# Kernel tuning notes

Measured on AMD Instinct MI355X. Metric: run time of the kernel, lower is better.

The kernel has to match this reference:

```python
import jax, jax.numpy as jnp
import numpy as np

K_BITS = 128  # hash bits (k in __init__)
WORD = 32     # pack bits into uint32 words -> K_BITS // WORD = 4 words


def _pack_bits(bits_u32):
    # bits_u32: [N, K_BITS] uint32 in {0,1} -> [N, K_BITS//WORD] uint32 keys
    N = bits_u32.shape[0]
    b = bits_u32.reshape(N, K_BITS // WORD, WORD)
    shifts = jnp.arange(WORD, dtype=jnp.uint32)
    return jnp.sum(jnp.left_shift(b, shifts), axis=-1, dtype=jnp.uint32)  # [N, 4]


def setup_inputs() -> dict:
    key = jax.random.key(0)
    k1, k2 = jax.random.split(key)
    T, B, D = 128, 64, 4096
    latent_state = jax.random.normal(k1, (T, B, D), dtype=jnp.float32)
    A = jax.random.normal(k2, (K_BITS, D), dtype=jnp.float32)  # fixed random projection buffer
    return {"latent_state": latent_state, "A": A}


def reference(latent_state, A):
    # latent_state: [T, B, D]; A: [k, D]. Returns intrinsic reward [T, B].
    T, B, D = latent_state.shape
    flat = latent_state.reshape(T * B, D)                    # detach is a no-op for fwd
    proj = flat @ A.T                                        # [N, k]
    bits = (proj > 0).astype(jnp.uint32)                     # SimHash sign bits
    words = _pack_bits(bits)                                 # [N, 4] collision-free 128-bit key

    # counts dict starts empty each run: visit count of row i is the number of
    # rows j <= i with an identical key (keys processed in row order).
    N = words.shape[0]
    eq = jnp.ones((N, N), dtype=bool)
    for w in range(K_BITS // WORD):  # small fixed loop over 4 key words
        eq = eq & (words[:, None, w] == words[None, :, w])
    counts = jnp.tril(eq).sum(axis=1)                        # [N] int, >= 1
    intrinsic = 1.0 / jnp.sqrt(counts.astype(latent_state.dtype))
    return intrinsic.reshape(T, B)
```

## Files before the change

### kernel.cpp

```cpp
#include <hip/hip_runtime.h>
#include <stdint.h>

#define D_DIM 4096
#define N_ROWS 8192

typedef __attribute__((ext_vector_type(8))) short bfrag8;
typedef __attribute__((ext_vector_type(4))) float facc4;

__device__ __forceinline__ uint32_t pack_bf16x2(float lo, float hi) {
    union { float f; uint32_t u; } a, b;
    a.f = lo; b.f = hi;
    return (b.u & 0xFFFF0000u) | (a.u >> 16);
}

__global__ void __launch_bounds__(256)
prep_A(const float* __restrict__ A, uint32_t* __restrict__ A_sw) {
    const int S = blockIdx.x * 256 + threadIdx.x;
    const int c = S >> 10;
    const int s = S & 1023;
    const int n = s >> 3;
    const int g = (s & 7) ^ (n & 7);
    const float* src = A + (size_t)n * D_DIM + c * 64 + g * 8;
    float4 f0 = *(const float4*)(src);
    float4 f1 = *(const float4*)(src + 4);
    uint4 o;
    o.x = pack_bf16x2(f0.x, f0.y);
    o.y = pack_bf16x2(f0.z, f0.w);
    o.z = pack_bf16x2(f1.x, f1.y);
    o.w = pack_bf16x2(f1.z, f1.w);
    *(uint4*)(A_sw + (size_t)S * 4) = o;
}

__global__ void __launch_bounds__(256)
gemm_pack(const float* __restrict__ L, const uint32_t* __restrict__ A_sw,
          unsigned long long* __restrict__ folded) {
    __shared__ ushort Ls[32 * 72];
    __shared__ uint4 As[1024];
    __shared__ unsigned long long halves[2][32];

    const int tid  = threadIdx.x;
    const int wave = tid >> 6;
    const int lane = tid & 63;
    const int row0 = blockIdx.x * 32;
    const int c  = lane & 15;
    const int q  = lane >> 4;
    const int wm = wave >> 1;
    const int wn = wave & 1;

    const int lrow = tid >> 3;
    const int lf4  = tid & 7;
    const float* lsrc = L + (size_t)(row0 + lrow) * D_DIM + lf4 * 4;
    ushort* ldst = &Ls[lrow * 72 + lf4 * 4];

    facc4 acc[4];
#pragma unroll
    for (int i = 0; i < 4; i++) acc[i] = (facc4){0.f, 0.f, 0.f, 0.f};

    for (int kc = 0; kc < D_DIM; kc += 64) {
        const uint32_t* gA = A_sw + (size_t)(kc >> 6) * 4096;
#pragma unroll
        for (int i = 0; i < 4; i++) {
            const int slot0 = wave * 256 + i * 64;
            __builtin_amdgcn_global_load_lds(
                (const __attribute__((address_space(1))) uint32_t*)(gA + (slot0 + lane) * 4),
                (__attribute__((address_space(3))) uint32_t*)(&As[slot0]),
                16, 0, 0);
        }
        float4 f0 = *(const float4*)(lsrc + kc);
        float4 f1 = *(const float4*)(lsrc + kc + 32);
        *(uint2*)ldst        = make_uint2(pack_bf16x2(f0.x, f0.y), pack_bf16x2(f0.z, f0.w));
        *(uint2*)(ldst + 32) = make_uint2(pack_bf16x2(f1.x, f1.y), pack_bf16x2(f1.z, f1.w));
        __syncthreads();

#pragma unroll
        for (int ks = 0; ks < 2; ks++) {
            bfrag8 a = *(const bfrag8*)&Ls[(16 * wm + c) * 72 + ks * 32 + q * 8];
#pragma unroll
            for (int ct = 0; ct < 4; ct++) {
                const int n  = 64 * wn + 16 * ct + c;
                const int gl = ks * 4 + q;
                bfrag8 b = *(const bfrag8*)&As[n * 8 + (gl ^ (n & 7))];
                acc[ct] = __builtin_amdgcn_mfma_f32_16x16x32_bf16(a, b, acc[ct], 0, 0, 0);
            }
        }
        __syncthreads();
    }

    unsigned long long masks[4][4];
#pragma unroll
    for (int ct = 0; ct < 4; ct++)
#pragma unroll
        for (int r = 0; r < 4; r++)
            masks[ct][r] = __ballot(acc[ct][r] > 0.0f);

    if (lane < 16) {
        const int qq = lane >> 2, r = lane & 3;
        unsigned long long half = 0;
#pragma unroll
        for (int ct = 0; ct < 4; ct++) {
            unsigned long long bits = (masks[ct][r] >> (16 * qq)) & 0xFFFFull;
            half |= bits << (16 * ct);
        }
        halves[wn][16 * wm + lane] = half;
    }
    __syncthreads();
    if (tid < 32)
        folded[row0 + tid] = halves[0][tid] ^ halves[1][tid];
}

__global__ void __launch_bounds__(256)
count_rows(const unsigned long long* __restrict__ folded, float* __restrict__ out) {
    const int row  = (blockIdx.x << 2) + (threadIdx.x >> 6);
    const int lane = threadIdx.x & 63;
    const unsigned long long my = folded[row];
    int cnt = 0;
    for (int j = lane; j <= row; j += 64)
        cnt += (folded[j] == my);
#pragma unroll
    for (int o = 32; o; o >>= 1) cnt += __shfl_xor(cnt, o, 64);
    if (lane == 0) out[row] = rsqrtf((float)cnt);
}

extern "C" void kernel_launch(void* const* d_in, const int* in_sizes, int n_in,
                              void* d_out, int out_size, void* d_ws, size_t ws_size,
                              hipStream_t stream) {
    const float* latent = (const float*)d_in[0];
    const float* A      = (const float*)d_in[1];
    float* out          = (float*)d_out;

    uint32_t* A_sw = (uint32_t*)d_ws;
    unsigned long long* folded = (unsigned long long*)((char*)d_ws + (1 << 20));

    prep_A<<<256, 256, 0, stream>>>(A, A_sw);
    gemm_pack<<<256, 256, 0, stream>>>(latent, A_sw, folded);
    count_rows<<<2048, 256, 0, stream>>>(folded, out);
}
```

Baseline: 256.0 us.

## Split GEMM over K across blocks and batch collision counting through LDS

Adds a split-K GEMM path. S blocks per 32-row tile write float partial projections to workspace, and a reduce kernel sums them, takes the sign bits and folds them into a key. The aim is to fill the GPU, which the 256-block launch leaves underused. The counting kernel is also rewritten: it stages all keys in LDS and has each wave handle four rows spread across the triangle, for shared loads and better load balance. The cost is extra global traffic for the partials (up to 32 MB) and one extra kernel launch. The split path only runs if the workspace is large enough.

Measured after the change: 226.3 us. -11.6%, faster.

```diff
diff --git a/kernel.cpp b/kernel.cpp
--- a/kernel.cpp
+++ b/kernel.cpp
@@ -6,6 +6,7 @@
 
 typedef __attribute__((ext_vector_type(8))) short bfrag8;
 typedef __attribute__((ext_vector_type(4))) float facc4;
+typedef unsigned long long u64;
 
 __device__ __forceinline__ uint32_t pack_bf16x2(float lo, float hi) {
     union { float f; uint32_t u; } a, b;
@@ -32,11 +33,93 @@
 }
 
 __global__ void __launch_bounds__(256)
-gemm_pack(const float* __restrict__ L, const uint32_t* __restrict__ A_sw,
-          unsigned long long* __restrict__ folded) {
+gemm_split(const float* __restrict__ L, const uint32_t* __restrict__ A_sw,
+           float* __restrict__ partials, int kpb) {
     __shared__ ushort Ls[32 * 72];
     __shared__ uint4 As[1024];
-    __shared__ unsigned long long halves[2][32];
+
+    const int tid  = threadIdx.x;
+    const int wave = tid >> 6;
+    const int lane = tid & 63;
+    const int split = blockIdx.x;
+    const int row0 = blockIdx.y * 32;
+    const int c  = lane & 15;
+    const int q  = lane >> 4;
+    const int wm = wave >> 1;
+    const int wn = wave & 1;
+
+    const int lrow = tid >> 3;
+    const int lf4  = tid & 7;
+    const float* lsrc = L + (size_t)(row0 + lrow) * D_DIM + lf4 * 4;
+    ushort* ldst = &Ls[lrow * 72 + lf4 * 4];
+
+    facc4 acc[4];
+#pragma unroll
+    for (int i = 0; i < 4; i++) acc[i] = (facc4){0.f, 0.f, 0.f, 0.f};
+
+    const int kc0 = split * kpb * 64;
+    const int kc1 = kc0 + kpb * 64;
+    for (int kc = kc0; kc < kc1; kc += 64) {
+        const uint32_t* gA = A_sw + (size_t)(kc >> 6) * 4096;
+#pragma unroll
+        for (int i = 0; i < 4; i++) {
+            const int slot0 = wave * 256 + i * 64;
+            __builtin_amdgcn_global_load_lds(
+                (const __attribute__((address_space(1))) uint32_t*)(gA + (slot0 + lane) * 4),
+                (__attribute__((address_space(3))) uint32_t*)(&As[slot0]),
+                16, 0, 0);
+        }
+        float4 f0 = *(const float4*)(lsrc + kc);
+        float4 f1 = *(const float4*)(lsrc + kc + 32);
+        *(uint2*)ldst        = make_uint2(pack_bf16x2(f0.x, f0.y), pack_bf16x2(f0.z, f0.w));
+        *(uint2*)(ldst + 32) = make_uint2(pack_bf16x2(f1.x, f1.y), pack_bf16x2(f1.z, f1.w));
+        __syncthreads();
+
+#pragma unroll
+        for (int ks = 0; ks < 2; ks++) {
+            bfrag8 a = *(const bfrag8*)&Ls[(16 * wm + c) * 72 + ks * 32 + q * 8];
+#pragma unroll
+            for (int ct = 0; ct < 4; ct++) {
+                const int n  = 64 * wn + 16 * ct + c;
+                const int gl = ks * 4 + q;
+                bfrag8 b = *(const bfrag8*)&As[n * 8 + (gl ^ (n & 7))];
+                acc[ct] = __builtin_amdgcn_mfma_f32_16x16x32_bf16(a, b, acc[ct], 0, 0, 0);
+            }
+        }
+        __syncthreads();
+    }
+
+    float* P = partials + ((size_t)split * N_ROWS * 128);
+    const int rb = row0 + 16 * wm + 4 * q;
+    const int cb = 64 * wn + c;
+#pragma unroll
+    for (int ct = 0; ct < 4; ct++)
+#pragma unroll
+        for (int r = 0; r < 4; r++)
+            P[(size_t)(rb + r) * 128 + cb + 16 * ct] = acc[ct][r];
+}
+
+__global__ void __launch_bounds__(256)
+reduce_pack(const float* __restrict__ partials, u64* __restrict__ folded, int S) {
+    const int row  = blockIdx.x * 4 + (threadIdx.x >> 6);
+    const int lane = threadIdx.x & 63;
+    float s0 = 0.f, s1 = 0.f;
+    for (int s = 0; s < S; s++) {
+        const float* P = partials + ((size_t)s * N_ROWS * 128) + (size_t)row * 128;
+        s0 += P[lane];
+        s1 += P[lane + 64];
+    }
+    u64 b0 = __ballot(s0 > 0.0f);
+    u64 b1 = __ballot(s1 > 0.0f);
+    if (lane == 0) folded[row] = b0 ^ b1;
+}
+
+__global__ void __launch_bounds__(256)
+gemm_pack(const float* __restrict__ L, const uint32_t* __restrict__ A_sw,
+          u64* __restrict__ folded) {
+    __shared__ ushort Ls[32 * 72];
+    __shared__ uint4 As[1024];
+    __shared__ u64 halves[2][32];
 
     const int tid  = threadIdx.x;
     const int wave = tid >> 6;
@@ -86,7 +169,7 @@
         __syncthreads();
     }
 
-    unsigned long long masks[4][4];
+    u64 masks[4][4];
 #pragma unroll
     for (int ct = 0; ct < 4; ct++)
 #pragma unroll
@@ -95,10 +178,10 @@
 
     if (lane < 16) {
         const int qq = lane >> 2, r = lane & 3;
-        unsigned long long half = 0;
+        u64 half = 0;
 #pragma unroll
         for (int ct = 0; ct < 4; ct++) {
-            unsigned long long bits = (masks[ct][r] >> (16 * qq)) & 0xFFFFull;
+            u64 bits = (masks[ct][r] >> (16 * qq)) & 0xFFFFull;
             half |= bits << (16 * ct);
         }
         halves[wn][16 * wm + lane] = half;
@@ -108,17 +191,37 @@
         folded[row0 + tid] = halves[0][tid] ^ halves[1][tid];
 }
 
-__global__ void __launch_bounds__(256)
-count_rows(const unsigned long long* __restrict__ folded, float* __restrict__ out) {
-    const int row  = (blockIdx.x << 2) + (threadIdx.x >> 6);
-    const int lane = threadIdx.x & 63;
-    const unsigned long long my = folded[row];
-    int cnt = 0;
-    for (int j = lane; j <= row; j += 64)
-        cnt += (folded[j] == my);
-#pragma unroll
-    for (int o = 32; o; o >>= 1) cnt += __shfl_xor(cnt, o, 64);
-    if (lane == 0) out[row] = rsqrtf((float)cnt);
+__global__ void __launch_bounds__(512)
+count_rows(const u64* __restrict__ folded, float* __restrict__ out) {
+    __shared__ u64 K[N_ROWS];
+    const int tid = threadIdx.x;
+    for (int i = tid; i < N_ROWS; i += 512) K[i] = folded[i];
+    __syncthreads();
+
+    const int g    = blockIdx.x * 8 + (tid >> 6);
+    const int lane = tid & 63;
+    int rows[4];
+    u64 my[4];
+    int cnt[4] = {0, 0, 0, 0};
+#pragma unroll
+    for (int r = 0; r < 4; r++) {
+        rows[r] = g + 2048 * r;
+        my[r] = K[rows[r]];
+    }
+    const int maxrow = rows[3];
+    for (int j = lane; j <= maxrow; j += 64) {
+        u64 k = K[j];
+#pragma unroll
+        for (int r = 0; r < 4; r++)
+            cnt[r] += (int)((j <= rows[r]) & (k == my[r]));
+    }
+#pragma unroll
+    for (int r = 0; r < 4; r++) {
+        int v = cnt[r];
+#pragma unroll
+        for (int o = 32; o; o >>= 1) v += __shfl_xor(v, o, 64);
+        if (lane == 0) out[rows[r]] = rsqrtf((float)v);
+    }
 }
 
 extern "C" void kernel_launch(void* const* d_in, const int* in_sizes, int n_in,
@@ -129,9 +232,22 @@
     float* out          = (float*)d_out;
 
     uint32_t* A_sw = (uint32_t*)d_ws;
-    unsigned long long* folded = (unsigned long long*)((char*)d_ws + (1 << 20));
+    u64* folded = (u64*)((char*)d_ws + (1 << 20));
+    float* partials = (float*)((char*)d_ws + (1 << 20) + (1 << 16));
+
+    const size_t base = (1 << 20) + (1 << 16);
+    const size_t per_split = (size_t)N_ROWS * 128 * sizeof(float);
+    int S = 0;
+    if (ws_size >= base + 8 * per_split)      S = 8;
+    else if (ws_size >= base + 4 * per_split) S = 4;
+    else if (ws_size >= base + 2 * per_split) S = 2;
 
     prep_A<<<256, 256, 0, stream>>>(A, A_sw);
-    gemm_pack<<<256, 256, 0, stream>>>(latent, A_sw, folded);
-    count_rows<<<2048, 256, 0, stream>>>(folded, out);
-}
+    if (S > 0) {
+        gemm_split<<<dim3(S, 256), 256, 0, stream>>>(latent, A_sw, partials, 64 / S);
+        reduce_pack<<<2048, 256, 0, stream>>>(partials, folded, S);
+    } else {
+        gemm_pack<<<256, 256, 0, stream>>>(latent, A_sw, folded);
+    }
+    count_rows<<<256, 512, 0, stream>>>(folded, out);
+}
```

## Split-K direct-register GEMM with partial reduction and LDS-cached collision counting

Applied to the files above, without the earlier changes.

Replaces the LDS-tiled GEMM with a per-wave kernel that loads latent rows straight into registers and reads a fragment-ordered bf16 image of A from global memory. The K dimension is split across up to 8 slices, chosen from the workspace size, so more waves run at once. A new reduce kernel sums the fp32 partials before taking sign bits and folding the hash. The counting kernel now stages all keys in shared memory and handles four rows per wave. The cost is extra global traffic to write and re-read the partials, plus one more kernel launch.

Result: faster. 240.9 us (-5.9%).

```diff
diff --git a/kernel.cpp b/kernel.cpp
--- a/kernel.cpp
+++ b/kernel.cpp
@@ -6,6 +6,7 @@
 
 typedef __attribute__((ext_vector_type(8))) short bfrag8;
 typedef __attribute__((ext_vector_type(4))) float facc4;
+typedef unsigned long long u64;
 
 __device__ __forceinline__ uint32_t pack_bf16x2(float lo, float hi) {
     union { float f; uint32_t u; } a, b;
@@ -14,13 +15,17 @@
 }
 
 __global__ void __launch_bounds__(256)
-prep_A(const float* __restrict__ A, uint32_t* __restrict__ A_sw) {
+prep_A(const float* __restrict__ A, uint32_t* __restrict__ Bimg) {
     const int S = blockIdx.x * 256 + threadIdx.x;
-    const int c = S >> 10;
-    const int s = S & 1023;
-    const int n = s >> 3;
-    const int g = (s & 7) ^ (n & 7);
-    const float* src = A + (size_t)n * D_DIM + c * 64 + g * 8;
+    const int chunk = S >> 10;
+    const int rest  = S & 1023;
+    const int tks   = rest >> 6;
+    const int lane  = rest & 63;
+    const int t  = tks >> 1;
+    const int ks = tks & 1;
+    const int c  = lane & 15;
+    const int q  = lane >> 4;
+    const float* src = A + (size_t)(16 * t + c) * D_DIM + chunk * 64 + ks * 32 + q * 8;
     float4 f0 = *(const float4*)(src);
     float4 f1 = *(const float4*)(src + 4);
     uint4 o;
@@ -28,97 +33,109 @@
     o.y = pack_bf16x2(f0.z, f0.w);
     o.z = pack_bf16x2(f1.x, f1.y);
     o.w = pack_bf16x2(f1.z, f1.w);
-    *(uint4*)(A_sw + (size_t)S * 4) = o;
+    *(uint4*)(Bimg + (size_t)S * 4) = o;
+}
+
+__global__ void __launch_bounds__(256, 3)
+gemm_direct(const float* __restrict__ L, const uint32_t* __restrict__ Bimg,
+            float* __restrict__ partials, int kpb) {
+    const int tid  = threadIdx.x;
+    const int lane = tid & 63;
+    const int gw   = blockIdx.x * 4 + (tid >> 6);
+    const int split = gw >> 9;
+    const int mwave = gw & 511;
+    const int c = lane & 15;
+    const int q = lane >> 4;
+
+    const float* lrow = L + (size_t)(16 * mwave + c) * D_DIM;
+
+    facc4 acc[8];
+#pragma unroll
+    for (int t = 0; t < 8; t++) acc[t] = (facc4){0.f, 0.f, 0.f, 0.f};
+
+    const int k0 = split * kpb;
+#pragma unroll 2
+    for (int k = k0; k < k0 + kpb; k++) {
+        const int kc = k * 64;
+        bfrag8 a[2];
+#pragma unroll
+        for (int ks = 0; ks < 2; ks++) {
+            const float* p = lrow + kc + ks * 32 + q * 8;
+            float4 f0 = *(const float4*)(p);
+            float4 f1 = *(const float4*)(p + 4);
+            uint4 u;
+            u.x = pack_bf16x2(f0.x, f0.y);
+            u.y = pack_bf16x2(f0.z, f0.w);
+            u.z = pack_bf16x2(f1.x, f1.y);
+            u.w = pack_bf16x2(f1.z, f1.w);
+            a[ks] = *(bfrag8*)&u;
+        }
+        const uint32_t* bbase = Bimg + ((size_t)k * 16) * 256 + lane * 4;
+#pragma unroll
+        for (int t = 0; t < 8; t++) {
+#pragma unroll
+            for (int ks = 0; ks < 2; ks++) {
+                bfrag8 b = *(const bfrag8*)(bbase + (t * 2 + ks) * 256);
+                acc[t] = __builtin_amdgcn_mfma_f32_16x16x32_bf16(a[ks], b, acc[t], 0, 0, 0);
+            }
+        }
+    }
+
+    float* P = partials + (size_t)split * N_ROWS * 128 + (size_t)(16 * mwave) * 128;
+#pragma unroll
+    for (int t = 0; t < 8; t++)
+#pragma unroll
+        for (int r = 0; r < 4; r++)
+            P[(4 * q + r) * 128 + 16 * t + c] = acc[t][r];
 }
 
 __global__ void __launch_bounds__(256)
-gemm_pack(const float* __restrict__ L, const uint32_t* __restrict__ A_sw,
-          unsigned long long* __restrict__ folded) {
-    __shared__ ushort Ls[32 * 72];
-    __shared__ uint4 As[1024];
-    __shared__ unsigned long long halves[2][32];
-
-    const int tid  = threadIdx.x;
-    const int wave = tid >> 6;
-    const int lane = tid & 63;
-    const int row0 = blockIdx.x * 32;
-    const int c  = lane & 15;
-    const int q  = lane >> 4;
-    const int wm = wave >> 1;
-    const int wn = wave & 1;
-
-    const int lrow = tid >> 3;
-    const int lf4  = tid & 7;
-    const float* lsrc = L + (size_t)(row0 + lrow) * D_DIM + lf4 * 4;
-    ushort* ldst = &Ls[lrow * 72 + lf4 * 4];
-
-    facc4 acc[4];
-#pragma unroll
-    for (int i = 0; i < 4; i++) acc[i] = (facc4){0.f, 0.f, 0.f, 0.f};
-
-    for (int kc = 0; kc < D_DIM; kc += 64) {
-        const uint32_t* gA = A_sw + (size_t)(kc >> 6) * 4096;
-#pragma unroll
-        for (int i = 0; i < 4; i++) {
-            const int slot0 = wave * 256 + i * 64;
-            __builtin_amdgcn_global_load_lds(
-                (const __attribute__((address_space(1))) uint32_t*)(gA + (slot0 + lane) * 4),
-                (__attribute__((address_space(3))) uint32_t*)(&As[slot0]),
-                16, 0, 0);
-        }
-        float4 f0 = *(const float4*)(lsrc + kc);
-        float4 f1 = *(const float4*)(lsrc + kc + 32);
-        *(uint2*)ldst        = make_uint2(pack_bf16x2(f0.x, f0.y), pack_bf16x2(f0.z, f0.w));
-        *(uint2*)(ldst + 32) = make_uint2(pack_bf16x2(f1.x, f1.y), pack_bf16x2(f1.z, f1.w));
-        __syncthreads();
-
-#pragma unroll
-        for (int ks = 0; ks < 2; ks++) {
-            bfrag8 a = *(const bfrag8*)&Ls[(16 * wm + c) * 72 + ks * 32 + q * 8];
-#pragma unroll
-            for (int ct = 0; ct < 4; ct++) {
-                const int n  = 64 * wn + 16 * ct + c;
-                const int gl = ks * 4 + q;
-                bfrag8 b = *(const bfrag8*)&As[n * 8 + (gl ^ (n & 7))];
-                acc[ct] = __builtin_amdgcn_mfma_f32_16x16x32_bf16(a, b, acc[ct], 0, 0, 0);
-            }
-        }
-        __syncthreads();
+reduce_pack(const float* __restrict__ partials, u64* __restrict__ folded, int S) {
+    const int row  = blockIdx.x * 4 + (threadIdx.x >> 6);
+    const int lane = threadIdx.x & 63;
+    float s0 = 0.f, s1 = 0.f;
+    for (int s = 0; s < S; s++) {
+        const float* P = partials + ((size_t)s * N_ROWS * 128) + (size_t)row * 128;
+        s0 += P[lane];
+        s1 += P[lane + 64];
     }
-
-    unsigned long long masks[4][4];
-#pragma unroll
-    for (int ct = 0; ct < 4; ct++)
-#pragma unroll
-        for (int r = 0; r < 4; r++)
-            masks[ct][r] = __ballot(acc[ct][r] > 0.0f);
-
-    if (lane < 16) {
-        const int qq = lane >> 2, r = lane & 3;
-        unsigned long long half = 0;
-#pragma unroll
-        for (int ct = 0; ct < 4; ct++) {
-            unsigned long long bits = (masks[ct][r] >> (16 * qq)) & 0xFFFFull;
-            half |= bits << (16 * ct);
-        }
-        halves[wn][16 * wm + lane] = half;
-    }
-    __syncthreads();
-    if (tid < 32)
-        folded[row0 + tid] = halves[0][tid] ^ halves[1][tid];
+    u64 b0 = __ballot(s0 > 0.0f);
+    u64 b1 = __ballot(s1 > 0.0f);
+    if (lane == 0) folded[row] = b0 ^ b1;
 }
 
 __global__ void __launch_bounds__(256)
-count_rows(const unsigned long long* __restrict__ folded, float* __restrict__ out) {
-    const int row  = (blockIdx.x << 2) + (threadIdx.x >> 6);
-    const int lane = threadIdx.x & 63;
-    const unsigned long long my = folded[row];
-    int cnt = 0;
-    for (int j = lane; j <= row; j += 64)
-        cnt += (folded[j] == my);
+count_rows(const u64* __restrict__ folded, float* __restrict__ out) {
+    __shared__ u64 K[N_ROWS];
+    const int tid = threadIdx.x;
+    for (int i = tid; i < N_ROWS / 2; i += 256)
+        ((uint4*)K)[i] = ((const uint4*)folded)[i];
+    __syncthreads();
+
+    const int g    = blockIdx.x * 4 + (tid >> 6);
+    const int lane = tid & 63;
+    int rows[4];
+    u64 my[4];
+    int cnt[4] = {0, 0, 0, 0};
 #pragma unroll
-    for (int o = 32; o; o >>= 1) cnt += __shfl_xor(cnt, o, 64);
-    if (lane == 0) out[row] = rsqrtf((float)cnt);
+    for (int r = 0; r < 4; r++) {
+        rows[r] = g + 2048 * r;
+        my[r] = K[rows[r]];
+    }
+    const int maxrow = rows[3];
+    for (int j = lane; j <= maxrow; j += 64) {
+        u64 k = K[j];
+#pragma unroll
+        for (int r = 0; r < 4; r++)
+            cnt[r] += (int)((j <= rows[r]) & (k == my[r]));
+    }
+#pragma unroll
+    for (int r = 0; r < 4; r++) {
+        int v = cnt[r];
+#pragma unroll
+        for (int o = 32; o; o >>= 1) v += __shfl_xor(v, o, 64);
+        if (lane == 0) out[rows[r]] = rsqrtf((float)v);
+    }
 }
 
 extern "C" void kernel_launch(void* const* d_in, const int* in_sizes, int n_in,
@@ -128,10 +145,19 @@
     const float* A      = (const float*)d_in[1];
     float* out          = (float*)d_out;
 
-    uint32_t* A_sw = (uint32_t*)d_ws;
-    unsigned long long* folded = (unsigned long long*)((char*)d_ws + (1 << 20));
+    uint32_t* Bimg = (uint32_t*)d_ws;
+    u64* folded = (u64*)((char*)d_ws + (1 << 20));
+    float* partials = (float*)((char*)d_ws + (1 << 20) + (1 << 16));
 
-    prep_A<<<256, 256, 0, stream>>>(A, A_sw);
-    gemm_pack<<<256, 256, 0, stream>>>(latent, A_sw, folded);
-    count_rows<<<2048, 256, 0, stream>>>(folded, out);
+    const size_t base = (1 << 20) + (1 << 16);
+    const size_t per_split = (size_t)N_ROWS * 128 * sizeof(float);
+    int S = 1;
+    if (ws_size >= base + 8 * per_split)      S = 8;
+    else if (ws_size >= base + 4 * per_split) S = 4;
+    else if (ws_size >= base + 2 * per_split) S = 2;
+
+    prep_A<<<256, 256, 0, stream>>>(A, Bimg);
+    gemm_direct<<<128 * S, 256, 0, stream>>>(latent, Bimg, partials, 64 / S);
+    reduce_pack<<<2048, 256, 0, stream>>>(partials, folded, S);
+    count_rows<<<512, 256, 0, stream>>>(folded, out);
 }
```
